# Kernel optimization log

Hardware: AMD Instinct MI355X
Metric: run time of the kernel (lower is better)

## Reference

```python
import jax, jax.numpy as jnp
import numpy as np

INV_SQRT2 = 0.7071067811865476
N, E, K, S = 10000, 120000, 8, 7
DE, DA, DT, DR, DC = 128, 128, 64, 16, 16
T = E * K

def act(x):
    return jax.nn.silu(x)

def residual_stack(x, Ws):
    # Ws: (n_layers, 2, D, D); GemNet ResidualLayer: two Dense+act, scaled skip
    for lw in Ws:
        y = act(act(x @ lw[0]) @ lw[1])
        x = (x + y) * INV_SQRT2
    return x

def bilinear(rbf_W1, sph, m, id_reduce, id_ragged, W):
    # EfficientInteractionBilinear (GemNet): ragged scatter into (E,Kmax,emb) then basis contractions
    m2 = jnp.zeros((rbf_W1.shape[0], sph.shape[1], m.shape[-1]), m.dtype)
    m2 = m2.at[id_reduce, id_ragged].set(m)          # (E, K, DT)
    sum_k = jnp.einsum('eks,ekc->esc', sph, m2)      # (E, S, DT)
    a = jnp.einsum('ejs,esc->ejc', rbf_W1, sum_k)    # (E, DC, DT)
    return jnp.einsum('ejc,cju->eu', a, W)           # (E, DT)

def _forward(h, m_st, rbf_h, rbf3, cbf_rbfW1, cbf_sph,
             W_mlp_st, W_m_kt, W_t_rbf, W_down, W_bil, W_st3, W_ts3,
             res_before, res_after, W_ae_rbf, W_ae_in, res_atom, W_asi, res_m,
             idx_s, idx_t, idx_swap, id3_kt, id3_st, id3_ragged_idx):
    x_skip = m_st @ W_mlp_st
    # --- TripletInteraction ---
    m_kt = act(m_st @ W_m_kt)
    m_kt = m_kt * (rbf3 @ W_t_rbf)        # scale_rbf == 1.0 (identity ScaleFactor)
    m_kt = act(m_kt @ W_down)             # (E, DT)
    xb = bilinear(cbf_rbfW1, cbf_sph, m_kt[id3_kt], id3_st, id3_ragged_idx, W_bil)
    x_st = act(xb @ W_st3)
    x_ts = act(xb @ W_ts3)[idx_swap]
    x3 = (x_st + x_ts) * INV_SQRT2
    # --- merge + residual stacks ---
    x = (x_skip + x3) * INV_SQRT2
    x = residual_stack(x, res_before)
    x = (x + m_st) * INV_SQRT2
    x = residual_stack(x, res_after)
    # --- AtomEmbedding: edge->atom scatter-add ---
    xa = x * (rbf_h @ W_ae_rbf)
    h2 = jax.ops.segment_sum(xa, idx_t, num_segments=h.shape[0])  # scale_sum == 1.0
    h_new = residual_stack(act(h2 @ W_ae_in), res_atom)
    # --- AtomSelfInteraction: gather-concat-Dense ---
    m = act(jnp.concatenate([h_new[idx_s], h_new[idx_t], x], axis=-1) @ W_asi)
    m = residual_stack(m, res_m)
    m = (m + x) * INV_SQRT2
    return h_new, m

def setup_inputs():
    key = jax.random.key(0)
    ks = jax.random.split(key, 24)
    def w(k, shape):
        return jax.random.normal(k, shape, jnp.float32) * (1.0 / np.sqrt(shape[-2]))
    return dict(
        h=jax.random.normal(ks[0], (N, DA), jnp.float32),
        m_st=jax.random.normal(ks[1], (E, DE), jnp.float32),
        rbf_h=jax.random.uniform(ks[2], (E, DR), jnp.float32),
        rbf3=jax.random.uniform(ks[3], (E, DR), jnp.float32),
        cbf_rbfW1=jax.random.normal(ks[4], (E, DC, S), jnp.float32) * 0.2,
        cbf_sph=jax.random.normal(ks[5], (E, K, S), jnp.float32) * 0.2,
        W_mlp_st=w(ks[6], (DE, DE)),
        W_m_kt=w(ks[7], (DE, DE)),
        W_t_rbf=w(ks[8], (DR, DE)),
        W_down=w(ks[9], (DE, DT)),
        W_bil=jax.random.normal(ks[10], (DT, DC, DT), jnp.float32) * (1.0 / np.sqrt(DT * DC)),
        W_st3=w(ks[11], (DT, DE)),
        W_ts3=w(ks[12], (DT, DE)),
        res_before=w(ks[13], (1, 2, DE, DE)),
        res_after=w(ks[14], (2, 2, DE, DE)),
        W_ae_rbf=w(ks[15], (DR, DE)),
        W_ae_in=w(ks[16], (DE, DA)),
        res_atom=w(ks[17], (2, 2, DA, DA)),
        W_asi=w(ks[18], (2 * DA + DE, DE)),
        res_m=w(ks[19], (2, 2, DE, DE)),
        idx_s=jax.random.randint(ks[20], (E,), 0, N, jnp.int32),
        idx_t=jax.random.randint(ks[21], (E,), 0, N, jnp.int32),
        idx_swap=jax.random.permutation(ks[22], E).astype(jnp.int32),
        id3_kt=jax.random.randint(ks[23], (T,), 0, E, jnp.int32),
        id3_st=jnp.repeat(jnp.arange(E, dtype=jnp.int32), K),
        id3_ragged_idx=jnp.tile(jnp.arange(K, dtype=jnp.int32), E),
    )

def reference(h, m_st, rbf_h, rbf3, cbf_rbfW1, cbf_sph,
              W_mlp_st, W_m_kt, W_t_rbf, W_down, W_bil, W_st3, W_ts3,
              res_before, res_after, W_ae_rbf, W_ae_in, res_atom, W_asi, res_m,
              idx_s, idx_t, idx_swap, id3_kt, id3_st, id3_ragged_idx):
    return _forward(h, m_st, rbf_h, rbf3, cbf_rbfW1, cbf_sph,
                    W_mlp_st, W_m_kt, W_t_rbf, W_down, W_bil, W_st3, W_ts3,
                    res_before, res_after, W_ae_rbf, W_ae_in, res_atom, W_asi, res_m,
                    idx_s, idx_t, idx_swap, id3_kt, id3_st, id3_ragged_idx)
```

## Files before the change

### kernel.cpp

```cpp
#include <hip/hip_runtime.h>


#define EE 120000
#define NA 10000

constexpr float C_INV = 0.70710678118654752440f;

using f32x4 = __attribute__((ext_vector_type(4))) float;
using f32x2 = __attribute__((ext_vector_type(2))) float;
using s16x8 = __attribute__((ext_vector_type(8))) short;
using s16x4 = __attribute__((ext_vector_type(4))) short;

__device__ __forceinline__ float act_silu(float x) { return x / (1.0f + __expf(-x)); }

__device__ __forceinline__ unsigned short f2bf(float f) {
    unsigned int u = __float_as_uint(f);
    u += 0x7fffu + ((u >> 16) & 1u);
    return (unsigned short)(u >> 16);
}
__device__ __forceinline__ float bf2f(unsigned short h) {
    return __uint_as_float(((unsigned int)h) << 16);
}
__device__ __forceinline__ unsigned int cvtpk(float a, float b) {
    unsigned int r;
    asm("v_cvt_pk_bf16_f32 %0, %1, %2" : "=v"(r) : "v"(a), "v"(b));
    return r;
}

template<int MT, int KQ>
__device__ __forceinline__ void load_w(const unsigned short* __restrict__ W, int KW,
                                       int l, s16x8 (&a)[MT][KQ])
{
    const int fr = l & 15;
    const int k8 = (l >> 4) << 3;
    #pragma unroll
    for (int mt = 0; mt < MT; ++mt)
        #pragma unroll
        for (int kq = 0; kq < KQ; ++kq)
            a[mt][kq] = *(const s16x8*)&W[(size_t)(mt * 16 + fr) * KW + kq * 32 + k8];
}

template<int MT, int NF, int KQ>
__device__ __forceinline__ void gemm_pre(
    const s16x8 (&a)[MT][KQ], const char* ldsB, int RS,
    int rowBase, int l, f32x4 (&acc)[MT][NF])
{
    const int fr = l & 15;
    const int k8 = (l >> 4) << 3;
    #pragma unroll
    for (int kq = 0; kq < KQ; ++kq) {
        s16x8 b[NF];
        #pragma unroll
        for (int nf = 0; nf < NF; ++nf) {
            const int row = rowBase + nf * 16 + fr;
            const int kb  = ((kq * 32 + k8) * 2) ^ ((row & 7) << 4);
            b[nf] = *(const s16x8*)(ldsB + row * RS + kb);
        }
        #pragma unroll
        for (int mt = 0; mt < MT; ++mt)
            #pragma unroll
            for (int nf = 0; nf < NF; ++nf)
                acc[mt][nf] = __builtin_amdgcn_mfma_f32_16x16x32_bf16(
                    a[mt][kq], b[nf], acc[mt][nf], 0, 0, 0);
    }
}

template<int MT, int NF>
__device__ __forceinline__ void zacc(f32x4 (&acc)[MT][NF])
{
    #pragma unroll
    for (int mt = 0; mt < MT; ++mt)
        #pragma unroll
        for (int nf = 0; nf < NF; ++nf)
            acc[mt][nf] = (f32x4){0.f, 0.f, 0.f, 0.f};
}

__device__ __forceinline__ void packA(char* lds, int RS, int row, int outF0, f32x4 v)
{
    uint2 p;
    p.x = cvtpk(v[0], v[1]);
    p.y = cvtpk(v[2], v[3]);
    *(uint2*)(lds + row * RS + ((outF0 * 2) ^ ((row & 7) << 4))) = p;
}

__device__ __forceinline__ void store_bf4(unsigned short* dst, f32x4 v)
{
    uint2 p;
    p.x = cvtpk(v[0], v[1]);
    p.y = cvtpk(v[2], v[3]);
    *(uint2*)dst = p;
}

template<int ROWS>
__device__ __forceinline__ void stage_f32(char* lds, const float* __restrict__ src,
                                          int row0, int M, int tid)
{
    #pragma unroll
    for (int u = 0; u < ROWS * 16 / 512; ++u) {
        const int flat = tid + u * 512;
        const int row  = flat >> 4;
        const int k8   = (flat & 15) << 3;
        const int grow = row0 + row;
        uint4 val = {0u, 0u, 0u, 0u};
        if (grow < M) {
            const float* p = src + (size_t)grow * 128 + k8;
            f32x4 lo = *(const f32x4*)p;
            f32x4 hi = *(const f32x4*)(p + 4);
            val.x = cvtpk(lo[0], lo[1]);
            val.y = cvtpk(lo[2], lo[3]);
            val.z = cvtpk(hi[0], hi[1]);
            val.w = cvtpk(hi[2], hi[3]);
        }
        *(uint4*)(lds + row * 256 + ((k8 * 2) ^ ((row & 7) << 4))) = val;
    }
}

template<bool MSTM, int NF>
__device__ __forceinline__ void res_layer(
    char* A, char* B,
    const unsigned short* W0, const unsigned short* W1,
    int wm, int wn, int l, f32x4 (&x)[2][NF],
    const s16x4 (*ms)[NF])
{
    const int fr = l & 15;
    const int fq = (l >> 4) << 2;

    s16x8 aw[2][4];
    load_w<2, 4>(W0 + (size_t)(wm * 32) * 128, 128, l, aw);
    f32x4 acc[2][NF];
    zacc(acc);
    gemm_pre<2, NF, 4>(aw, A, 256, wn * NF * 16, l, acc);

    s16x8 aw1[2][4];
    load_w<2, 4>(W1 + (size_t)(wm * 32) * 128, 128, l, aw1);

    #pragma unroll
    for (int mt = 0; mt < 2; ++mt)
        #pragma unroll
        for (int nf = 0; nf < NF; ++nf) {
            const int row = wn * NF * 16 + nf * 16 + fr;
            const int of0 = wm * 32 + mt * 16 + fq;
            f32x4 v;
            #pragma unroll
            for (int q = 0; q < 4; ++q) v[q] = act_silu(acc[mt][nf][q]);
            packA(B, 256, row, of0, v);
        }
    __syncthreads();

    zacc(acc);
    gemm_pre<2, NF, 4>(aw1, B, 256, wn * NF * 16, l, acc);
    #pragma unroll
    for (int mt = 0; mt < 2; ++mt)
        #pragma unroll
        for (int nf = 0; nf < NF; ++nf) {
            const int row = wn * NF * 16 + nf * 16 + fr;
            const int of0 = wm * 32 + mt * 16 + fq;
            #pragma unroll
            for (int q = 0; q < 4; ++q)
                x[mt][nf][q] = (x[mt][nf][q] + act_silu(acc[mt][nf][q])) * C_INV;
            if (MSTM) {
                #pragma unroll
                for (int q = 0; q < 4; ++q)
                    x[mt][nf][q] = (x[mt][nf][q] +
                                    bf2f((unsigned short)ms[mt][nf][q])) * C_INV;
            }
            packA(A, 256, row, of0, x[mt][nf]);
        }
    __syncthreads();
}

__device__ __forceinline__ s16x4 read_frag(const char* lds, int row, int of0)
{
    return *(const s16x4*)(lds + row * 256 + ((of0 * 2) ^ ((row & 7) << 4)));
}

__global__ __launch_bounds__(512, 4) void front_k(
    const float* __restrict__ m_st, const unsigned short* __restrict__ scale_b,
    const unsigned short* __restrict__ Wmkt, const unsigned short* __restrict__ Wdown,
    unsigned short* __restrict__ mkt_b)
{
    __shared__ char A[128 * 256];
    const int tid = threadIdx.x;
    const int l = tid & 63, w = tid >> 6, wm = w & 3, wn = w >> 2;
    const int fr = l & 15, fq = (l >> 4) << 2;
    const int row0 = blockIdx.x * 128;

    s16x8 aw[2][4];
    load_w<2, 4>(Wmkt + (size_t)(wm * 32) * 128, 128, l, aw);

    stage_f32<128>(A, m_st, row0, EE, tid);
    __syncthreads();

    f32x4 acc[2][4];
    zacc(acc);
    gemm_pre<2, 4, 4>(aw, A, 256, wn * 64, l, acc);

    s16x8 aw2[1][4];
    load_w<1, 4>(Wdown + (size_t)(wm * 16) * 128, 128, l, aw2);

    __syncthreads();
    #pragma unroll
    for (int mt = 0; mt < 2; ++mt)
        #pragma unroll
        for (int nf = 0; nf < 4; ++nf) {
            const int row = wn * 64 + nf * 16 + fr;
            const int grow = row0 + row;
            const int of0 = wm * 32 + mt * 16 + fq;
            f32x4 v = {0.f, 0.f, 0.f, 0.f};
            if (grow < EE) {
                s16x4 sc = *(const s16x4*)&scale_b[(size_t)grow * 128 + of0];
                #pragma unroll
                for (int q = 0; q < 4; ++q)
                    v[q] = act_silu(acc[mt][nf][q]) * bf2f((unsigned short)sc[q]);
            }
            packA(A, 256, row, of0, v);
        }
    __syncthreads();

    f32x4 acc2[1][4];
    zacc(acc2);
    gemm_pre<1, 4, 4>(aw2, A, 256, wn * 64, l, acc2);
    #pragma unroll
    for (int nf = 0; nf < 4; ++nf) {
        const int row = wn * 64 + nf * 16 + fr;
        const int grow = row0 + row;
        if (grow >= EE) continue;
        const int of0 = wm * 16 + fq;
        f32x4 v;
        #pragma unroll
        for (int q = 0; q < 4; ++q) v[q] = act_silu(acc2[0][nf][q]);
        store_bf4(&mkt_b[(size_t)grow * 64 + of0], v);
    }
}

__global__ __launch_bounds__(512, 4) void st3ts3_k(
    const unsigned short* __restrict__ xb_b,
    const unsigned short* __restrict__ Wst3, const unsigned short* __restrict__ Wts3,
    unsigned short* __restrict__ yst, unsigned short* __restrict__ yts)
{
    __shared__ char A[128 * 128];
    const int tid = threadIdx.x;
    const int l = tid & 63, w = tid >> 6, wm = w & 3, wn = w >> 2;
    const int fr = l & 15, fq = (l >> 4) << 2;
    const int row0 = blockIdx.x * 128;

    s16x8 awS[2][2], awT[2][2];
    load_w<2, 2>(Wst3 + (size_t)(wm * 32) * 64, 64, l, awS);
    load_w<2, 2>(Wts3 + (size_t)(wm * 32) * 64, 64, l, awT);

    #pragma unroll
    for (int u = 0; u < 2; ++u) {
        const int flat = tid + u * 512;
        const int row = flat >> 3;
        const int k8 = (flat & 7) << 3;
        const int grow = row0 + row;
        s16x8 v = {0, 0, 0, 0, 0, 0, 0, 0};
        if (grow < EE) v = *(const s16x8*)&xb_b[(size_t)grow * 64 + k8];
        *(s16x8*)(A + row * 128 + ((k8 * 2) ^ ((row & 7) << 4))) = v;
    }
    __syncthreads();

    f32x4 aS[2][4], aT[2][4];
    zacc(aS); zacc(aT);
    {
        const int k8 = (l >> 4) << 3;
        #pragma unroll
        for (int kq = 0; kq < 2; ++kq) {
            s16x8 b[4];
            #pragma unroll
            for (int nf = 0; nf < 4; ++nf) {
                const int row = wn * 64 + nf * 16 + fr;
                const int kb  = ((kq * 32 + k8) * 2) ^ ((row & 7) << 4);
                b[nf] = *(const s16x8*)(A + row * 128 + kb);
            }
            #pragma unroll
            for (int mt = 0; mt < 2; ++mt)
                #pragma unroll
                for (int nf = 0; nf < 4; ++nf) {
                    aS[mt][nf] = __builtin_amdgcn_mfma_f32_16x16x32_bf16(
                        awS[mt][kq], b[nf], aS[mt][nf], 0, 0, 0);
                    aT[mt][nf] = __builtin_amdgcn_mfma_f32_16x16x32_bf16(
                        awT[mt][kq], b[nf], aT[mt][nf], 0, 0, 0);
                }
        }
    }

    #pragma unroll
    for (int mt = 0; mt < 2; ++mt)
        #pragma unroll
        for (int nf = 0; nf < 4; ++nf) {
            const int row = wn * 64 + nf * 16 + fr;
            const int grow = row0 + row;
            if (grow >= EE) continue;
            const int of0 = wm * 32 + mt * 16 + fq;
            f32x4 vs, vt;
            #pragma unroll
            for (int q = 0; q < 4; ++q) {
                vs[q] = act_silu(aS[mt][nf][q]);
                vt[q] = act_silu(aT[mt][nf][q]);
            }
            store_bf4(&yst[(size_t)grow * 128 + of0], vs);
            store_bf4(&yts[(size_t)grow * 128 + of0], vt);
        }
}

__global__ __launch_bounds__(512, 4) void chain_k(
    const float* __restrict__ m_st,
    const unsigned short* __restrict__ yst, const unsigned short* __restrict__ yts,
    const int* __restrict__ idx_swap,
    const unsigned short* __restrict__ Wmlp,
    const unsigned short* __restrict__ Wrb0, const unsigned short* __restrict__ Wrb1,
    const unsigned short* __restrict__ Wra0, const unsigned short* __restrict__ Wra1,
    const unsigned short* __restrict__ Wra2, const unsigned short* __restrict__ Wra3,
    unsigned short* __restrict__ xb_out)
{
    __shared__ char A[128 * 256];
    __shared__ char B[128 * 256];
    const int tid = threadIdx.x;
    const int l = tid & 63, w = tid >> 6, wm = w & 3, wn = w >> 2;
    const int fr = l & 15, fq = (l >> 4) << 2;
    const int row0 = blockIdx.x * 128;

    s16x8 aw[2][4];
    load_w<2, 4>(Wmlp + (size_t)(wm * 32) * 128, 128, l, aw);

    stage_f32<128>(A, m_st, row0, EE, tid);
    __syncthreads();

    f32x4 acc[2][4];
    zacc(acc);
    gemm_pre<2, 4, 4>(aw, A, 256, wn * 64, l, acc);

    s16x4 ms[2][4];
    #pragma unroll
    for (int mt = 0; mt < 2; ++mt)
        #pragma unroll
        for (int nf = 0; nf < 4; ++nf)
            ms[mt][nf] = read_frag(A, wn * 64 + nf * 16 + fr, wm * 32 + mt * 16 + fq);

    f32x4 x[2][4];
    #pragma unroll
    for (int mt = 0; mt < 2; ++mt)
        #pragma unroll
        for (int nf = 0; nf < 4; ++nf) {
            const int row = wn * 64 + nf * 16 + fr;
            const int grow = row0 + row;
            const int of0 = wm * 32 + mt * 16 + fq;
            if (grow < EE) {
                s16x4 a = *(const s16x4*)&yst[(size_t)grow * 128 + of0];
                const int sw = idx_swap[grow];
                s16x4 b = *(const s16x4*)&yts[(size_t)sw * 128 + of0];
                #pragma unroll
                for (int q = 0; q < 4; ++q)
                    x[mt][nf][q] = (acc[mt][nf][q] +
                        (bf2f((unsigned short)a[q]) + bf2f((unsigned short)b[q])) * C_INV) * C_INV;
            } else {
                x[mt][nf] = (f32x4){0.f, 0.f, 0.f, 0.f};
            }
        }
    __syncthreads();
    #pragma unroll
    for (int mt = 0; mt < 2; ++mt)
        #pragma unroll
        for (int nf = 0; nf < 4; ++nf)
            packA(A, 256, wn * 64 + nf * 16 + fr, wm * 32 + mt * 16 + fq, x[mt][nf]);
    __syncthreads();

    res_layer<true , 4>(A, B, Wrb0, Wrb1, wm, wn, l, x, ms);
    res_layer<false, 4>(A, B, Wra0, Wra1, wm, wn, l, x, nullptr);
    res_layer<false, 4>(A, B, Wra2, Wra3, wm, wn, l, x, nullptr);

    #pragma unroll
    for (int mt = 0; mt < 2; ++mt)
        #pragma unroll
        for (int nf = 0; nf < 4; ++nf) {
            const int row = wn * 64 + nf * 16 + fr;
            const int grow = row0 + row;
            if (grow >= EE) continue;
            const int of0 = wm * 32 + mt * 16 + fq;
            store_bf4(&xb_out[(size_t)grow * 128 + of0], x[mt][nf]);
        }
}

__global__ __launch_bounds__(512, 4) void atom_k(
    const float* __restrict__ h2,
    const unsigned short* __restrict__ Wae,
    const unsigned short* __restrict__ Wr0, const unsigned short* __restrict__ Wr1,
    const unsigned short* __restrict__ Wr2, const unsigned short* __restrict__ Wr3,
    float* __restrict__ out_h, unsigned short* __restrict__ h_b)
{
    __shared__ char A[64 * 256];
    __shared__ char B[64 * 256];
    const int tid = threadIdx.x;
    const int l = tid & 63, w = tid >> 6, wm = w & 3, wn = w >> 2;
    const int fr = l & 15, fq = (l >> 4) << 2;
    const int row0 = blockIdx.x * 64;

    s16x8 aw[2][4];
    load_w<2, 4>(Wae + (size_t)(wm * 32) * 128, 128, l, aw);

    stage_f32<64>(A, h2, row0, NA, tid);
    __syncthreads();

    f32x4 acc[2][2];
    zacc(acc);
    gemm_pre<2, 2, 4>(aw, A, 256, wn * 32, l, acc);
    f32x4 x[2][2];
    #pragma unroll
    for (int mt = 0; mt < 2; ++mt)
        #pragma unroll
        for (int nf = 0; nf < 2; ++nf)
            #pragma unroll
            for (int q = 0; q < 4; ++q)
                x[mt][nf][q] = act_silu(acc[mt][nf][q]);
    __syncthreads();
    #pragma unroll
    for (int mt = 0; mt < 2; ++mt)
        #pragma unroll
        for (int nf = 0; nf < 2; ++nf)
            packA(A, 256, wn * 32 + nf * 16 + fr, wm * 32 + mt * 16 + fq, x[mt][nf]);
    __syncthreads();

    res_layer<false, 2>(A, B, Wr0, Wr1, wm, wn, l, x, nullptr);
    res_layer<false, 2>(A, B, Wr2, Wr3, wm, wn, l, x, nullptr);

    #pragma unroll
    for (int mt = 0; mt < 2; ++mt)
        #pragma unroll
        for (int nf = 0; nf < 2; ++nf) {
            const int row = wn * 32 + nf * 16 + fr;
            const int grow = row0 + row;
            if (grow >= NA) continue;
            const int of0 = wm * 32 + mt * 16 + fq;
            *(f32x4*)&out_h[(size_t)grow * 128 + of0] = x[mt][nf];
            store_bf4(&h_b[(size_t)grow * 128 + of0], x[mt][nf]);
        }
}

__global__ __launch_bounds__(512, 4) void asi_k(
    const unsigned short* __restrict__ h_b, const unsigned short* __restrict__ x_b,
    const int* __restrict__ idx_s, const int* __restrict__ idx_t,
    const unsigned short* __restrict__ Wasi,
    const unsigned short* __restrict__ Wm0, const unsigned short* __restrict__ Wm1,
    const unsigned short* __restrict__ Wm2, const unsigned short* __restrict__ Wm3,
    float* __restrict__ out_m)
{
    __shared__ char A[128 * 256];
    __shared__ char B[128 * 256];
    const int tid = threadIdx.x;
    const int l = tid & 63, w = tid >> 6, wm = w & 3, wn = w >> 2;
    const int fr = l & 15, fq = (l >> 4) << 2;
    const int row0 = blockIdx.x * 128;

    f32x4 acc[2][4];
    zacc(acc);

    for (int c = 0; c < 3; ++c) {
        s16x8 aw[2][4];
        load_w<2, 4>(Wasi + (size_t)(wm * 32) * 384 + c * 128, 384, l, aw);
        #pragma unroll
        for (int u = 0; u < 4; ++u) {
            const int flat = tid + u * 512;
            const int row = flat >> 4;
            const int k8 = (flat & 15) << 3;
            const int grow = row0 + row;
            s16x8 v = {0, 0, 0, 0, 0, 0, 0, 0};
            if (grow < EE) {
                const unsigned short* src =
                    (c == 0) ? h_b + (size_t)idx_s[grow] * 128
                  : (c == 1) ? h_b + (size_t)idx_t[grow] * 128
                             : x_b + (size_t)grow * 128;
                v = *(const s16x8*)&src[k8];
            }
            *(s16x8*)(A + row * 256 + ((k8 * 2) ^ ((row & 7) << 4))) = v;
        }
        __syncthreads();
        gemm_pre<2, 4, 4>(aw, A, 256, wn * 64, l, acc);
        __syncthreads();
    }

    f32x4 x[2][4];
    #pragma unroll
    for (int mt = 0; mt < 2; ++mt)
        #pragma unroll
        for (int nf = 0; nf < 4; ++nf)
            #pragma unroll
            for (int q = 0; q < 4; ++q)
                x[mt][nf][q] = act_silu(acc[mt][nf][q]);
    #pragma unroll
    for (int mt = 0; mt < 2; ++mt)
        #pragma unroll
        for (int nf = 0; nf < 4; ++nf)
            packA(A, 256, wn * 64 + nf * 16 + fr, wm * 32 + mt * 16 + fq, x[mt][nf]);
    __syncthreads();

    res_layer<false, 4>(A, B, Wm0, Wm1, wm, wn, l, x, nullptr);
    res_layer<false, 4>(A, B, Wm2, Wm3, wm, wn, l, x, nullptr);

    #pragma unroll
    for (int mt = 0; mt < 2; ++mt)
        #pragma unroll
        for (int nf = 0; nf < 4; ++nf) {
            const int row = wn * 64 + nf * 16 + fr;
            const int grow = row0 + row;
            if (grow >= EE) continue;
            const int of0 = wm * 32 + mt * 16 + fq;
            s16x4 xv = *(const s16x4*)&x_b[(size_t)grow * 128 + of0];
            f32x4 o;
            #pragma unroll
            for (int q = 0; q < 4; ++q)
                o[q] = (x[mt][nf][q] + bf2f((unsigned short)xv[q])) * C_INV;
            *(f32x4*)&out_m[(size_t)grow * 128 + of0] = o;
        }
}

__global__ __launch_bounds__(256) void rbf_scale_k(
    const float* __restrict__ A, const float* __restrict__ W,
    unsigned short* __restrict__ out, int M)
{
    __shared__ float Ws[16][128];
    const int tid = threadIdx.x;
    #pragma unroll
    for (int t = tid; t < 512; t += 256) {
        int kk = t >> 5, c4 = (t & 31) << 2;
        *(float4*)&Ws[kk][c4] = *(const float4*)(W + kk * 128 + c4);
    }
    __syncthreads();
    const int tx = tid & 31, ty = tid >> 5;
    const int row0 = blockIdx.x * 128;
    #pragma unroll
    for (int i = 0; i < 16; ++i) {
        const int row = row0 + ty + i * 8;
        if (row >= M) continue;
        float av[16];
        #pragma unroll
        for (int j = 0; j < 4; ++j) {
            float4 a = *(const float4*)(A + (size_t)row * 16 + j * 4);
            av[j * 4] = a.x; av[j * 4 + 1] = a.y; av[j * 4 + 2] = a.z; av[j * 4 + 3] = a.w;
        }
        f32x4 s = {0.f, 0.f, 0.f, 0.f};
        #pragma unroll
        for (int k = 0; k < 16; ++k) {
            float4 wv = *(const float4*)&Ws[k][tx * 4];
            s[0] += av[k] * wv.x; s[1] += av[k] * wv.y;
            s[2] += av[k] * wv.z; s[3] += av[k] * wv.w;
        }
        store_bf4(&out[(size_t)row * 128 + tx * 4], s);
    }
}

__global__ void hist_k(const int* __restrict__ idxt, int* __restrict__ cnt)
{
    int i = blockIdx.x * 256 + threadIdx.x;
    if (i < EE) atomicAdd(&cnt[idxt[i]], 1);
}

__global__ __launch_bounds__(256) void scan_k(const int* __restrict__ cnt,
                                              int* __restrict__ start, int* __restrict__ wrk)
{
    __shared__ int ps[256];
    const int t = threadIdx.x;
    int s = 0;
    for (int j = 0; j < 40; ++j) {
        int idx = t * 40 + j;
        if (idx < NA) s += cnt[idx];
    }
    ps[t] = s;
    __syncthreads();
    for (int off = 1; off < 256; off <<= 1) {
        int v = (t >= off) ? ps[t - off] : 0;
        __syncthreads();
        ps[t] += v;
        __syncthreads();
    }
    int run = ps[t] - s;
    for (int j = 0; j < 40; ++j) {
        int idx = t * 40 + j;
        if (idx < NA) {
            start[idx] = run;
            wrk[idx] = run;
            run += cnt[idx];
        }
    }
    if (t == 255) start[NA] = ps[255];
}

__global__ void place_k(const int* __restrict__ idxt, int* __restrict__ wrk,
                        int* __restrict__ order)
{
    int i = blockIdx.x * 256 + threadIdx.x;
    if (i < EE) {
        int pos = atomicAdd(&wrk[idxt[i]], 1);
        order[pos] = i;
    }
}

__global__ __launch_bounds__(256) void segsum_k(
    const unsigned short* __restrict__ x_b, const float* __restrict__ rbf_h,
    const float* __restrict__ Wae, const int* __restrict__ start,
    const int* __restrict__ order, float* __restrict__ h2)
{
    const int tid = threadIdx.x;
    const int l = tid & 63, w = tid >> 6;
    const int a = blockIdx.x * 4 + w;
    if (a >= NA) return;

    float wc[32];
    #pragma unroll
    for (int j = 0; j < 16; ++j) {
        f32x2 v = *(const f32x2*)(Wae + j * 128 + 2 * l);
        wc[2 * j] = v[0]; wc[2 * j + 1] = v[1];
    }

    const int s = start[a], e_end = start[a + 1];
    float acc0 = 0.f, acc1 = 0.f;
    for (int i = s; i < e_end; ++i) {
        const int e = __builtin_amdgcn_readfirstlane(order[i]);
        const unsigned int xv = *(const unsigned int*)(x_b + (size_t)e * 128 + 2 * l);
        const float* rp = rbf_h + (size_t)e * 16;
        float c0 = 0.f, c1 = 0.f;
        #pragma unroll
        for (int j = 0; j < 16; ++j) {
            float r = rp[j];
            c0 += r * wc[2 * j];
            c1 += r * wc[2 * j + 1];
        }
        acc0 += bf2f((unsigned short)(xv & 0xffff)) * c0;
        acc1 += bf2f((unsigned short)(xv >> 16)) * c1;
    }
    f32x2 o; o[0] = acc0; o[1] = acc1;
    *(f32x2*)&h2[(size_t)a * 128 + 2 * l] = o;
}

__global__ void wconv_k(const float* __restrict__ Wbil, unsigned short* __restrict__ WT)
{
    int t = blockIdx.x * 256 + threadIdx.x;
    int u = t >> 10, k = t & 1023, j = k >> 6, c = k & 63;
    WT[t] = f2bf(Wbil[(size_t)(c * 16 + j) * 64 + u]);
}

struct WDesc { const float* src; int K; int N; int off; };
struct WTab  { WDesc d[21]; };

__global__ void wconvall_k(WTab tab, unsigned short* __restrict__ dst)
{
    WDesc d = tab.d[blockIdx.x];
    const int tot = d.K * d.N;
    for (int i = threadIdx.x; i < tot; i += 256) {
        int n = i / d.K, k = i - n * d.K;
        dst[d.off + i] = f2bf(d.src[(size_t)k * d.N + n]);
    }
}

__device__ __forceinline__ float rlc(const f32x4& cv, int idx, int lbase)
{
    const int c = idx & 3;
    float comp = (c == 0) ? cv[0] : (c == 1) ? cv[1] : (c == 2) ? cv[2] : cv[3];
    return __uint_as_float(__builtin_amdgcn_readlane(__float_as_uint(comp),
                                                     lbase + (idx >> 2)));
}

__global__ __launch_bounds__(512) void bilinear3_k(
    const unsigned short* __restrict__ mkt,
    const float* __restrict__ rbfW1,
    const float* __restrict__ sph,
    const int*   __restrict__ id3kt,
    const unsigned short* __restrict__ WT,
    unsigned short* __restrict__ xb)
{
    __shared__ unsigned short aS[32 * 1024];
    float* pS = (float*)aS;

    const int tid = threadIdx.x;
    const int l   = tid & 63;
    const int w   = tid >> 6;
    const int e0  = blockIdx.x * 32;

    s16x8 bfrag[4][4];
    {
        const int u  = l & 15;
        const int kh = w * 128 + ((l >> 4) << 3);
        #pragma unroll
        for (int nt = 0; nt < 4; ++nt)
            #pragma unroll
            for (int kq = 0; kq < 4; ++kq)
                bfrag[nt][kq] = *(const s16x8*)&WT[(size_t)(nt * 16 + u) * 1024 + kh + kq * 32];
    }

    #pragma unroll
    for (int r = 0; r < 4; ++r) {
        const int eL = r * 8 + w;
        const int eG = e0 + eL;

        f32x4 cv = {0.f, 0.f, 0.f, 0.f};
        if (l < 14)       cv = *(const f32x4*)(sph   + (size_t)eG * 56  + l * 4);
        else if (l < 42)  cv = *(const f32x4*)(rbfW1 + (size_t)eG * 112 + (l - 14) * 4);

        float m2r[8];
        #pragma unroll
        for (int k = 0; k < 8; ++k)
            m2r[k] = bf2f(mkt[(size_t)id3kt[eG * 8 + k] * 64 + l]);

        float sk[7] = {0.f, 0.f, 0.f, 0.f, 0.f, 0.f, 0.f};
        #pragma unroll
        for (int k = 0; k < 8; ++k)
            #pragma unroll
            for (int s = 0; s < 7; ++s)
                sk[s] += rlc(cv, k * 7 + s, 0) * m2r[k];

        unsigned short* arow = aS + eL * 1024;
        const int lsw = l ^ ((eL & 7) << 3);
        #pragma unroll
        for (int j = 0; j < 16; ++j) {
            float av = 0.f;
            #pragma unroll
            for (int s = 0; s < 7; ++s)
                av += rlc(cv, j * 7 + s, 14) * sk[s];
            arow[j * 64 + lsw] = f2bf(av);
        }
    }
    __syncthreads();

    f32x4 acc[2][4];
    #pragma unroll
    for (int mt = 0; mt < 2; ++mt)
        #pragma unroll
        for (int nt = 0; nt < 4; ++nt)
            acc[mt][nt] = (f32x4){0.f, 0.f, 0.f, 0.f};

    const int kbase = w * 128 + ((l >> 4) << 3);
    #pragma unroll
    for (int kq = 0; kq < 4; ++kq) {
        s16x8 afr[2];
        #pragma unroll
        for (int mt = 0; mt < 2; ++mt) {
            const int row = mt * 16 + (l & 15);
            const int kk  = (kbase + kq * 32) ^ ((row & 7) << 3);
            afr[mt] = *(const s16x8*)&aS[row * 1024 + kk];
        }
        #pragma unroll
        for (int mt = 0; mt < 2; ++mt)
            #pragma unroll
            for (int nt = 0; nt < 4; ++nt)
                acc[mt][nt] = __builtin_amdgcn_mfma_f32_16x16x32_bf16(
                    afr[mt], bfrag[nt][kq], acc[mt][nt], 0, 0, 0);
    }
    __syncthreads();

    #pragma unroll
    for (int mt = 0; mt < 2; ++mt)
        #pragma unroll
        for (int nt = 0; nt < 4; ++nt)
            #pragma unroll
            for (int q = 0; q < 4; ++q) {
                const int e = mt * 16 + ((l >> 4) << 2) + q;
                const int u = nt * 16 + (l & 15);
                pS[(w * 32 + e) * 64 + u] = acc[mt][nt][q];
            }
    __syncthreads();

    {
        const int e  = tid >> 4;
        const int u0 = (tid & 15) << 2;
        f32x4 s = (f32x4){0.f, 0.f, 0.f, 0.f};
        #pragma unroll
        for (int ww = 0; ww < 8; ++ww)
            s += *(const f32x4*)&pS[(ww * 32 + e) * 64 + u0];
        store_bf4(&xb[(size_t)(e0 + e) * 64 + u0], s);
    }
}

extern "C" void kernel_launch(void* const* d_in, const int* in_sizes, int n_in,
                              void* d_out, int out_size, void* d_ws, size_t ws_size,
                              hipStream_t stream)
{
    const float* m_st      = (const float*)d_in[1];
    const float* rbf_h     = (const float*)d_in[2];
    const float* rbf3      = (const float*)d_in[3];
    const float* cbf_rbfW1 = (const float*)d_in[4];
    const float* cbf_sph   = (const float*)d_in[5];
    const float* W_mlp_st  = (const float*)d_in[6];
    const float* W_m_kt    = (const float*)d_in[7];
    const float* W_t_rbf   = (const float*)d_in[8];
    const float* W_down    = (const float*)d_in[9];
    const float* W_bil     = (const float*)d_in[10];
    const float* W_st3     = (const float*)d_in[11];
    const float* W_ts3     = (const float*)d_in[12];
    const float* resb      = (const float*)d_in[13];
    const float* resa      = (const float*)d_in[14];
    const float* W_ae_rbf  = (const float*)d_in[15];
    const float* W_ae_in   = (const float*)d_in[16];
    const float* resat     = (const float*)d_in[17];
    const float* W_asi     = (const float*)d_in[18];
    const float* resm      = (const float*)d_in[19];
    const int*   idx_s     = (const int*)d_in[20];
    const int*   idx_t     = (const int*)d_in[21];
    const int*   idx_swap  = (const int*)d_in[22];
    const int*   id3_kt    = (const int*)d_in[23];

    float* h2 = (float*)d_ws;
    unsigned short* scale_b = (unsigned short*)(h2 + (size_t)NA * 128);
    unsigned short* yst_b   = scale_b;
    unsigned short* yts_b   = scale_b + (size_t)EE * 128;
    unsigned short* x_b     = yts_b + (size_t)EE * 128;
    unsigned short* mkt_b   = x_b + (size_t)EE * 128;
    unsigned short* xb_b    = mkt_b + (size_t)EE * 64;
    unsigned short* h_b     = xb_b + (size_t)EE * 64;
    unsigned short* WTbil   = h_b + (size_t)NA * 128;
    unsigned short* WTall   = WTbil + 65536;
    int* cnt   = (int*)(WTall + 352256);
    int* start = cnt + NA;
    int* wrk   = start + NA + 1;
    int* order = wrk + NA;

    float* out_h = (float*)d_out;
    float* out_m = out_h + (size_t)NA * 128;

    const dim3 blk(256);
    const dim3 blk5(512);
    const int gE  = (EE + 127) / 128;
    const int gN64 = (NA + 63) / 64;
    constexpr size_t SQ = 128 * 128;

    WTab tab; int off = 0; int oi = 0;
    auto put = [&](const float* s, int K, int N) {
        int o = off; tab.d[oi].src = s; tab.d[oi].K = K; tab.d[oi].N = N;
        tab.d[oi].off = o; ++oi; off += K * N; return o;
    };
    const int o_mlp  = put(W_mlp_st, 128, 128);
    const int o_mktw = put(W_m_kt, 128, 128);
    const int o_down = put(W_down, 128, 64);
    const int o_st3  = put(W_st3, 64, 128);
    const int o_ts3  = put(W_ts3, 64, 128);
    const int o_rb0  = put(resb, 128, 128);
    const int o_rb1  = put(resb + SQ, 128, 128);
    const int o_ra0  = put(resa, 128, 128);
    const int o_ra1  = put(resa + SQ, 128, 128);
    const int o_ra2  = put(resa + 2 * SQ, 128, 128);
    const int o_ra3  = put(resa + 3 * SQ, 128, 128);
    const int o_aein = put(W_ae_in, 128, 128);
    const int o_rat0 = put(resat, 128, 128);
    const int o_rat1 = put(resat + SQ, 128, 128);
    const int o_rat2 = put(resat + 2 * SQ, 128, 128);
    const int o_rat3 = put(resat + 3 * SQ, 128, 128);
    const int o_asi  = put(W_asi, 384, 128);
    const int o_rm0  = put(resm, 128, 128);
    const int o_rm1  = put(resm + SQ, 128, 128);
    const int o_rm2  = put(resm + 2 * SQ, 128, 128);
    const int o_rm3  = put(resm + 3 * SQ, 128, 128);

    hipMemsetAsync(cnt, 0, NA * sizeof(int), stream);
    wconv_k<<<65536 / 256, blk, 0, stream>>>(W_bil, WTbil);
    wconvall_k<<<21, blk, 0, stream>>>(tab, WTall);
    hist_k<<<(EE + 255) / 256, blk, 0, stream>>>(idx_t, cnt);
    scan_k<<<1, blk, 0, stream>>>(cnt, start, wrk);
    place_k<<<(EE + 255) / 256, blk, 0, stream>>>(idx_t, wrk, order);

    rbf_scale_k<<<gE, blk, 0, stream>>>(rbf3, W_t_rbf, scale_b, EE);
    front_k<<<gE, blk5, 0, stream>>>(m_st, scale_b, WTall + o_mktw, WTall + o_down, mkt_b);
    bilinear3_k<<<EE / 32, blk5, 0, stream>>>(
        mkt_b, cbf_rbfW1, cbf_sph, id3_kt, WTbil, xb_b);
    st3ts3_k<<<gE, blk5, 0, stream>>>(xb_b, WTall + o_st3, WTall + o_ts3, yst_b, yts_b);
    chain_k<<<gE, blk5, 0, stream>>>(
        m_st, yst_b, yts_b, idx_swap,
        WTall + o_mlp, WTall + o_rb0, WTall + o_rb1,
        WTall + o_ra0, WTall + o_ra1, WTall + o_ra2, WTall + o_ra3,
        x_b);
    segsum_k<<<(NA + 3) / 4, blk, 0, stream>>>(x_b, rbf_h, W_ae_rbf, start, order, h2);
    atom_k<<<gN64, blk5, 0, stream>>>(
        h2, WTall + o_aein,
        WTall + o_rat0, WTall + o_rat1, WTall + o_rat2, WTall + o_rat3,
        out_h, h_b);
    asi_k<<<gE, blk5, 0, stream>>>(
        h_b, x_b, idx_s, idx_t,
        WTall + o_asi,
        WTall + o_rm0, WTall + o_rm1, WTall + o_rm2, WTall + o_rm3,
        out_m);
}
```

Baseline: 701.7 us.

## Halve row tiles, raise occupancy, and restructure bilinear kernel with scalar coefficient loads

Most edge kernels (front, st3ts3, chain, asi) now process 64 rows per block instead of 128, with half the LDS and accumulators, and request 8 blocks per CU in their launch bounds. This should raise occupancy and latency hiding. The bilinear kernel now handles 16 edges per block. It reads the sph and rbf coefficients through wave-uniform scalar addresses instead of readlane, and loads W_bil fragments from global memory inside the MFMA loop instead of holding them in registers. In exchange there are twice as many blocks and weight-fragment loads per row, and the tighter register budget risks spills.

```diff
diff --git a/kernel.cpp b/kernel.cpp
--- a/kernel.cpp
+++ b/kernel.cpp
@@ -174,26 +174,26 @@
     return *(const s16x4*)(lds + row * 256 + ((of0 * 2) ^ ((row & 7) << 4)));
 }
 
-__global__ __launch_bounds__(512, 4) void front_k(
+__global__ __launch_bounds__(512, 8) void front_k(
     const float* __restrict__ m_st, const unsigned short* __restrict__ scale_b,
     const unsigned short* __restrict__ Wmkt, const unsigned short* __restrict__ Wdown,
     unsigned short* __restrict__ mkt_b)
 {
-    __shared__ char A[128 * 256];
+    __shared__ char A[64 * 256];
     const int tid = threadIdx.x;
     const int l = tid & 63, w = tid >> 6, wm = w & 3, wn = w >> 2;
     const int fr = l & 15, fq = (l >> 4) << 2;
-    const int row0 = blockIdx.x * 128;
+    const int row0 = blockIdx.x * 64;
 
     s16x8 aw[2][4];
     load_w<2, 4>(Wmkt + (size_t)(wm * 32) * 128, 128, l, aw);
 
-    stage_f32<128>(A, m_st, row0, EE, tid);
-    __syncthreads();
-
-    f32x4 acc[2][4];
+    stage_f32<64>(A, m_st, row0, EE, tid);
+    __syncthreads();
+
+    f32x4 acc[2][2];
     zacc(acc);
-    gemm_pre<2, 4, 4>(aw, A, 256, wn * 64, l, acc);
+    gemm_pre<2, 2, 4>(aw, A, 256, wn * 32, l, acc);
 
     s16x8 aw2[1][4];
     load_w<1, 4>(Wdown + (size_t)(wm * 16) * 128, 128, l, aw2);
@@ -202,8 +202,8 @@
     #pragma unroll
     for (int mt = 0; mt < 2; ++mt)
         #pragma unroll
-        for (int nf = 0; nf < 4; ++nf) {
-            const int row = wn * 64 + nf * 16 + fr;
+        for (int nf = 0; nf < 2; ++nf) {
+            const int row = wn * 32 + nf * 16 + fr;
             const int grow = row0 + row;
             const int of0 = wm * 32 + mt * 16 + fq;
             f32x4 v = {0.f, 0.f, 0.f, 0.f};
@@ -217,12 +217,12 @@
         }
     __syncthreads();
 
-    f32x4 acc2[1][4];
+    f32x4 acc2[1][2];
     zacc(acc2);
-    gemm_pre<1, 4, 4>(aw2, A, 256, wn * 64, l, acc2);
-    #pragma unroll
-    for (int nf = 0; nf < 4; ++nf) {
-        const int row = wn * 64 + nf * 16 + fr;
+    gemm_pre<1, 2, 4>(aw2, A, 256, wn * 32, l, acc2);
+    #pragma unroll
+    for (int nf = 0; nf < 2; ++nf) {
+        const int row = wn * 32 + nf * 16 + fr;
         const int grow = row0 + row;
         if (grow >= EE) continue;
         const int of0 = wm * 16 + fq;
@@ -233,26 +233,24 @@
     }
 }
 
-__global__ __launch_bounds__(512, 4) void st3ts3_k(
+__global__ __launch_bounds__(512, 8) void st3ts3_k(
     const unsigned short* __restrict__ xb_b,
     const unsigned short* __restrict__ Wst3, const unsigned short* __restrict__ Wts3,
     unsigned short* __restrict__ yst, unsigned short* __restrict__ yts)
 {
-    __shared__ char A[128 * 128];
+    __shared__ char A[64 * 128];
     const int tid = threadIdx.x;
     const int l = tid & 63, w = tid >> 6, wm = w & 3, wn = w >> 2;
     const int fr = l & 15, fq = (l >> 4) << 2;
-    const int row0 = blockIdx.x * 128;
+    const int row0 = blockIdx.x * 64;
 
     s16x8 awS[2][2], awT[2][2];
     load_w<2, 2>(Wst3 + (size_t)(wm * 32) * 64, 64, l, awS);
     load_w<2, 2>(Wts3 + (size_t)(wm * 32) * 64, 64, l, awT);
 
-    #pragma unroll
-    for (int u = 0; u < 2; ++u) {
-        const int flat = tid + u * 512;
-        const int row = flat >> 3;
-        const int k8 = (flat & 7) << 3;
+    {
+        const int row = tid >> 3;
+        const int k8 = (tid & 7) << 3;
         const int grow = row0 + row;
         s16x8 v = {0, 0, 0, 0, 0, 0, 0, 0};
         if (grow < EE) v = *(const s16x8*)&xb_b[(size_t)grow * 64 + k8];
@@ -260,23 +258,23 @@
     }
     __syncthreads();
 
-    f32x4 aS[2][4], aT[2][4];
+    f32x4 aS[2][2], aT[2][2];
     zacc(aS); zacc(aT);
     {
         const int k8 = (l >> 4) << 3;
         #pragma unroll
         for (int kq = 0; kq < 2; ++kq) {
-            s16x8 b[4];
-            #pragma unroll
-            for (int nf = 0; nf < 4; ++nf) {
-                const int row = wn * 64 + nf * 16 + fr;
+            s16x8 b[2];
+            #pragma unroll
+            for (int nf = 0; nf < 2; ++nf) {
+                const int row = wn * 32 + nf * 16 + fr;
                 const int kb  = ((kq * 32 + k8) * 2) ^ ((row & 7) << 4);
                 b[nf] = *(const s16x8*)(A + row * 128 + kb);
             }
             #pragma unroll
             for (int mt = 0; mt < 2; ++mt)
                 #pragma unroll
-                for (int nf = 0; nf < 4; ++nf) {
+                for (int nf = 0; nf < 2; ++nf) {
                     aS[mt][nf] = __builtin_amdgcn_mfma_f32_16x16x32_bf16(
                         awS[mt][kq], b[nf], aS[mt][nf], 0, 0, 0);
                     aT[mt][nf] = __builtin_amdgcn_mfma_f32_16x16x32_bf16(
@@ -288,8 +286,8 @@
     #pragma unroll
     for (int mt = 0; mt < 2; ++mt)
         #pragma unroll
-        for (int nf = 0; nf < 4; ++nf) {
-            const int row = wn * 64 + nf * 16 + fr;
+        for (int nf = 0; nf < 2; ++nf) {
+            const int row = wn * 32 + nf * 16 + fr;
             const int grow = row0 + row;
             if (grow >= EE) continue;
             const int of0 = wm * 32 + mt * 16 + fq;
@@ -304,7 +302,7 @@
         }
 }
 
-__global__ __launch_bounds__(512, 4) void chain_k(
+__global__ __launch_bounds__(512, 8) void chain_k(
     const float* __restrict__ m_st,
     const unsigned short* __restrict__ yst, const unsigned short* __restrict__ yts,
     const int* __restrict__ idx_swap,
@@ -314,36 +312,36 @@
     const unsigned short* __restrict__ Wra2, const unsigned short* __restrict__ Wra3,
     unsigned short* __restrict__ xb_out)
 {
-    __shared__ char A[128 * 256];
-    __shared__ char B[128 * 256];
+    __shared__ char A[64 * 256];
+    __shared__ char B[64 * 256];
     const int tid = threadIdx.x;
     const int l = tid & 63, w = tid >> 6, wm = w & 3, wn = w >> 2;
     const int fr = l & 15, fq = (l >> 4) << 2;
-    const int row0 = blockIdx.x * 128;
+    const int row0 = blockIdx.x * 64;
 
     s16x8 aw[2][4];
     load_w<2, 4>(Wmlp + (size_t)(wm * 32) * 128, 128, l, aw);
 
-    stage_f32<128>(A, m_st, row0, EE, tid);
-    __syncthreads();
-
-    f32x4 acc[2][4];
+    stage_f32<64>(A, m_st, row0, EE, tid);
+    __syncthreads();
+
+    f32x4 acc[2][2];
     zacc(acc);
-    gemm_pre<2, 4, 4>(aw, A, 256, wn * 64, l, acc);
-
-    s16x4 ms[2][4];
-    #pragma unroll
-    for (int mt = 0; mt < 2; ++mt)
-        #pragma unroll
-        for (int nf = 0; nf < 4; ++nf)
-            ms[mt][nf] = read_frag(A, wn * 64 + nf * 16 + fr, wm * 32 + mt * 16 + fq);
-
-    f32x4 x[2][4];
-    #pragma unroll
-    for (int mt = 0; mt < 2; ++mt)
-        #pragma unroll
-        for (int nf = 0; nf < 4; ++nf) {
-            const int row = wn * 64 + nf * 16 + fr;
+    gemm_pre<2, 2, 4>(aw, A, 256, wn * 32, l, acc);
+
+    s16x4 ms[2][2];
+    #pragma unroll
+    for (int mt = 0; mt < 2; ++mt)
+        #pragma unroll
+        for (int nf = 0; nf < 2; ++nf)
+            ms[mt][nf] = read_frag(A, wn * 32 + nf * 16 + fr, wm * 32 + mt * 16 + fq);
+
+    f32x4 x[2][2];
+    #pragma unroll
+    for (int mt = 0; mt < 2; ++mt)
+        #pragma unroll
+        for (int nf = 0; nf < 2; ++nf) {
+            const int row = wn * 32 + nf * 16 + fr;
             const int grow = row0 + row;
             const int of0 = wm * 32 + mt * 16 + fq;
             if (grow < EE) {
@@ -362,19 +360,19 @@
     #pragma unroll
     for (int mt = 0; mt < 2; ++mt)
         #pragma unroll
-        for (int nf = 0; nf < 4; ++nf)
-            packA(A, 256, wn * 64 + nf * 16 + fr, wm * 32 + mt * 16 + fq, x[mt][nf]);
-    __syncthreads();
-
-    res_layer<true , 4>(A, B, Wrb0, Wrb1, wm, wn, l, x, ms);
-    res_layer<false, 4>(A, B, Wra0, Wra1, wm, wn, l, x, nullptr);
-    res_layer<false, 4>(A, B, Wra2, Wra3, wm, wn, l, x, nullptr);
-
-    #pragma unroll
-    for (int mt = 0; mt < 2; ++mt)
-        #pragma unroll
-        for (int nf = 0; nf < 4; ++nf) {
-            const int row = wn * 64 + nf * 16 + fr;
+        for (int nf = 0; nf < 2; ++nf)
+            packA(A, 256, wn * 32 + nf * 16 + fr, wm * 32 + mt * 16 + fq, x[mt][nf]);
+    __syncthreads();
+
+    res_layer<true , 2>(A, B, Wrb0, Wrb1, wm, wn, l, x, ms);
+    res_layer<false, 2>(A, B, Wra0, Wra1, wm, wn, l, x, nullptr);
+    res_layer<false, 2>(A, B, Wra2, Wra3, wm, wn, l, x, nullptr);
+
+    #pragma unroll
+    for (int mt = 0; mt < 2; ++mt)
+        #pragma unroll
+        for (int nf = 0; nf < 2; ++nf) {
+            const int row = wn * 32 + nf * 16 + fr;
             const int grow = row0 + row;
             if (grow >= EE) continue;
             const int of0 = wm * 32 + mt * 16 + fq;
@@ -382,7 +380,7 @@
         }
 }
 
-__global__ __launch_bounds__(512, 4) void atom_k(
+__global__ __launch_bounds__(512, 8) void atom_k(
     const float* __restrict__ h2,
     const unsigned short* __restrict__ Wae,
     const unsigned short* __restrict__ Wr0, const unsigned short* __restrict__ Wr1,
@@ -437,7 +435,7 @@
         }
 }
 
-__global__ __launch_bounds__(512, 4) void asi_k(
+__global__ __launch_bounds__(512, 8) void asi_k(
     const unsigned short* __restrict__ h_b, const unsigned short* __restrict__ x_b,
     const int* __restrict__ idx_s, const int* __restrict__ idx_t,
     const unsigned short* __restrict__ Wasi,
@@ -445,21 +443,21 @@
     const unsigned short* __restrict__ Wm2, const unsigned short* __restrict__ Wm3,
     float* __restrict__ out_m)
 {
-    __shared__ char A[128 * 256];
-    __shared__ char B[128 * 256];
+    __shared__ char A[64 * 256];
+    __shared__ char B[64 * 256];
     const int tid = threadIdx.x;
     const int l = tid & 63, w = tid >> 6, wm = w & 3, wn = w >> 2;
     const int fr = l & 15, fq = (l >> 4) << 2;
-    const int row0 = blockIdx.x * 128;
-
-    f32x4 acc[2][4];
+    const int row0 = blockIdx.x * 64;
+
+    f32x4 acc[2][2];
     zacc(acc);
 
     for (int c = 0; c < 3; ++c) {
         s16x8 aw[2][4];
         load_w<2, 4>(Wasi + (size_t)(wm * 32) * 384 + c * 128, 384, l, aw);
         #pragma unroll
-        for (int u = 0; u < 4; ++u) {
+        for (int u = 0; u < 2; ++u) {
             const int flat = tid + u * 512;
             const int row = flat >> 4;
             const int k8 = (flat & 15) << 3;
@@ -475,33 +473,33 @@
             *(s16x8*)(A + row * 256 + ((k8 * 2) ^ ((row & 7) << 4))) = v;
         }
         __syncthreads();
-        gemm_pre<2, 4, 4>(aw, A, 256, wn * 64, l, acc);
+        gemm_pre<2, 2, 4>(aw, A, 256, wn * 32, l, acc);
         __syncthreads();
     }
 
-    f32x4 x[2][4];
-    #pragma unroll
-    for (int mt = 0; mt < 2; ++mt)
-        #pragma unroll
-        for (int nf = 0; nf < 4; ++nf)
+    f32x4 x[2][2];
+    #pragma unroll
+    for (int mt = 0; mt < 2; ++mt)
+        #pragma unroll
+        for (int nf = 0; nf < 2; ++nf)
             #pragma unroll
             for (int q = 0; q < 4; ++q)
                 x[mt][nf][q] = act_silu(acc[mt][nf][q]);
     #pragma unroll
     for (int mt = 0; mt < 2; ++mt)
         #pragma unroll
-        for (int nf = 0; nf < 4; ++nf)
-            packA(A, 256, wn * 64 + nf * 16 + fr, wm * 32 + mt * 16 + fq, x[mt][nf]);
-    __syncthreads();
-
-    res_layer<false, 4>(A, B, Wm0, Wm1, wm, wn, l, x, nullptr);
-    res_layer<false, 4>(A, B, Wm2, Wm3, wm, wn, l, x, nullptr);
-
-    #pragma unroll
-    for (int mt = 0; mt < 2; ++mt)
-        #pragma unroll
-        for (int nf = 0; nf < 4; ++nf) {
-            const int row = wn * 64 + nf * 16 + fr;
+        for (int nf = 0; nf < 2; ++nf)
+            packA(A, 256, wn * 32 + nf * 16 + fr, wm * 32 + mt * 16 + fq, x[mt][nf]);
+    __syncthreads();
+
+    res_layer<false, 2>(A, B, Wm0, Wm1, wm, wn, l, x, nullptr);
+    res_layer<false, 2>(A, B, Wm2, Wm3, wm, wn, l, x, nullptr);
+
+    #pragma unroll
+    for (int mt = 0; mt < 2; ++mt)
+        #pragma unroll
+        for (int nf = 0; nf < 2; ++nf) {
+            const int row = wn * 32 + nf * 16 + fr;
             const int grow = row0 + row;
             if (grow >= EE) continue;
             const int of0 = wm * 32 + mt * 16 + fq;
@@ -652,15 +650,7 @@
     }
 }
 
-__device__ __forceinline__ float rlc(const f32x4& cv, int idx, int lbase)
-{
-    const int c = idx & 3;
-    float comp = (c == 0) ? cv[0] : (c == 1) ? cv[1] : (c == 2) ? cv[2] : cv[3];
-    return __uint_as_float(__builtin_amdgcn_readlane(__float_as_uint(comp),
-                                                     lbase + (idx >> 2)));
-}
-
-__global__ __launch_bounds__(512) void bilinear3_k(
+__global__ __launch_bounds__(512, 8) void bilinear4_k(
     const unsigned short* __restrict__ mkt,
     const float* __restrict__ rbfW1,
     const float* __restrict__ sph,
@@ -668,45 +658,34 @@
     const unsigned short* __restrict__ WT,
     unsigned short* __restrict__ xb)
 {
-    __shared__ unsigned short aS[32 * 1024];
+    __shared__ unsigned short aS[16 * 1024];
     float* pS = (float*)aS;
 
     const int tid = threadIdx.x;
     const int l   = tid & 63;
     const int w   = tid >> 6;
-    const int e0  = blockIdx.x * 32;
-
-    s16x8 bfrag[4][4];
-    {
-        const int u  = l & 15;
-        const int kh = w * 128 + ((l >> 4) << 3);
-        #pragma unroll
-        for (int nt = 0; nt < 4; ++nt)
-            #pragma unroll
-            for (int kq = 0; kq < 4; ++kq)
-                bfrag[nt][kq] = *(const s16x8*)&WT[(size_t)(nt * 16 + u) * 1024 + kh + kq * 32];
-    }
-
-    #pragma unroll
-    for (int r = 0; r < 4; ++r) {
+    const int e0  = blockIdx.x * 16;
+
+    #pragma unroll
+    for (int r = 0; r < 2; ++r) {
         const int eL = r * 8 + w;
-        const int eG = e0 + eL;
-
-        f32x4 cv = {0.f, 0.f, 0.f, 0.f};
-        if (l < 14)       cv = *(const f32x4*)(sph   + (size_t)eG * 56  + l * 4);
-        else if (l < 42)  cv = *(const f32x4*)(rbfW1 + (size_t)eG * 112 + (l - 14) * 4);
+        const int eU = __builtin_amdgcn_readfirstlane(e0 + eL);
+
+        const int*   idU = id3kt + (size_t)eU * 8;
+        const float* spU = sph   + (size_t)eU * 56;
+        const float* rbU = rbfW1 + (size_t)eU * 112;
 
         float m2r[8];
         #pragma unroll
         for (int k = 0; k < 8; ++k)
-            m2r[k] = bf2f(mkt[(size_t)id3kt[eG * 8 + k] * 64 + l]);
+            m2r[k] = bf2f(mkt[(size_t)idU[k] * 64 + l]);
 
         float sk[7] = {0.f, 0.f, 0.f, 0.f, 0.f, 0.f, 0.f};
         #pragma unroll
         for (int k = 0; k < 8; ++k)
             #pragma unroll
             for (int s = 0; s < 7; ++s)
-                sk[s] += rlc(cv, k * 7 + s, 0) * m2r[k];
+                sk[s] += spU[k * 7 + s] * m2r[k];
 
         unsigned short* arow = aS + eL * 1024;
         const int lsw = l ^ ((eL & 7) << 3);
@@ -715,58 +694,50 @@
             float av = 0.f;
             #pragma unroll
             for (int s = 0; s < 7; ++s)
-                av += rlc(cv, j * 7 + s, 14) * sk[s];
+                av += rbU[j * 7 + s] * sk[s];
             arow[j * 64 + lsw] = f2bf(av);
         }
     }
     __syncthreads();
 
-    f32x4 acc[2][4];
-    #pragma unroll
-    for (int mt = 0; mt < 2; ++mt)
-        #pragma unroll
-        for (int nt = 0; nt < 4; ++nt)
-            acc[mt][nt] = (f32x4){0.f, 0.f, 0.f, 0.f};
-
+    f32x4 acc[4];
+    #pragma unroll
+    for (int nt = 0; nt < 4; ++nt) acc[nt] = (f32x4){0.f, 0.f, 0.f, 0.f};
+
+    const int u16   = l & 15;
     const int kbase = w * 128 + ((l >> 4) << 3);
     #pragma unroll
     for (int kq = 0; kq < 4; ++kq) {
-        s16x8 afr[2];
-        #pragma unroll
-        for (int mt = 0; mt < 2; ++mt) {
-            const int row = mt * 16 + (l & 15);
-            const int kk  = (kbase + kq * 32) ^ ((row & 7) << 3);
-            afr[mt] = *(const s16x8*)&aS[row * 1024 + kk];
-        }
-        #pragma unroll
-        for (int mt = 0; mt < 2; ++mt)
-            #pragma unroll
-            for (int nt = 0; nt < 4; ++nt)
-                acc[mt][nt] = __builtin_amdgcn_mfma_f32_16x16x32_bf16(
-                    afr[mt], bfrag[nt][kq], acc[mt][nt], 0, 0, 0);
-    }
-    __syncthreads();
-
-    #pragma unroll
-    for (int mt = 0; mt < 2; ++mt)
-        #pragma unroll
-        for (int nt = 0; nt < 4; ++nt)
-            #pragma unroll
-            for (int q = 0; q < 4; ++q) {
-                const int e = mt * 16 + ((l >> 4) << 2) + q;
-                const int u = nt * 16 + (l & 15);
-                pS[(w * 32 + e) * 64 + u] = acc[mt][nt][q];
-            }
+        const int row = l & 15;
+        const int kk  = (kbase + kq * 32) ^ ((row & 7) << 3);
+        s16x8 afr = *(const s16x8*)&aS[row * 1024 + kk];
+        #pragma unroll
+        for (int nt = 0; nt < 4; ++nt) {
+            s16x8 bfr = *(const s16x8*)&WT[(size_t)(nt * 16 + u16) * 1024 + kbase + kq * 32];
+            acc[nt] = __builtin_amdgcn_mfma_f32_16x16x32_bf16(afr, bfr, acc[nt], 0, 0, 0);
+        }
+    }
+    __syncthreads();
+
+    #pragma unroll
+    for (int nt = 0; nt < 4; ++nt)
+        #pragma unroll
+        for (int q = 0; q < 4; ++q) {
+            const int e = ((l >> 4) << 2) + q;
+            const int u = nt * 16 + (l & 15);
+            pS[(w * 16 + e) * 64 + u] = acc[nt][q];
+        }
     __syncthreads();
 
     {
-        const int e  = tid >> 4;
-        const int u0 = (tid & 15) << 2;
-        f32x4 s = (f32x4){0.f, 0.f, 0.f, 0.f};
+        const int e  = tid >> 5;
+        const int u0 = (tid & 31) << 1;
+        f32x2 s = (f32x2){0.f, 0.f};
         #pragma unroll
         for (int ww = 0; ww < 8; ++ww)
-            s += *(const f32x4*)&pS[(ww * 32 + e) * 64 + u0];
-        store_bf4(&xb[(size_t)(e0 + e) * 64 + u0], s);
+            s += *(const f32x2*)&pS[(ww * 16 + e) * 64 + u0];
+        unsigned int pk = cvtpk(s[0], s[1]);
+        *(unsigned int*)&xb[(size_t)(e0 + e) * 64 + u0] = pk;
     }
 }
 
@@ -818,8 +789,9 @@
 
     const dim3 blk(256);
     const dim3 blk5(512);
-    const int gE  = (EE + 127) / 128;
-    const int gN64 = (NA + 63) / 64;
+    const int gE128 = (EE + 127) / 128;
+    const int gE64  = (EE + 63) / 64;
+    const int gN64  = (NA + 63) / 64;
     constexpr size_t SQ = 128 * 128;
 
     WTab tab; int off = 0; int oi = 0;
@@ -856,12 +828,12 @@
     scan_k<<<1, blk, 0, stream>>>(cnt, start, wrk);
     place_k<<<(EE + 255) / 256, blk, 0, stream>>>(idx_t, wrk, order);
 
-    rbf_scale_k<<<gE, blk, 0, stream>>>(rbf3, W_t_rbf, scale_b, EE);
-    front_k<<<gE, blk5, 0, stream>>>(m_st, scale_b, WTall + o_mktw, WTall + o_down, mkt_b);
-    bilinear3_k<<<EE / 32, blk5, 0, stream>>>(
+    rbf_scale_k<<<gE128, blk, 0, stream>>>(rbf3, W_t_rbf, scale_b, EE);
+    front_k<<<gE64, blk5, 0, stream>>>(m_st, scale_b, WTall + o_mktw, WTall + o_down, mkt_b);
+    bilinear4_k<<<EE / 16, blk5, 0, stream>>>(
         mkt_b, cbf_rbfW1, cbf_sph, id3_kt, WTbil, xb_b);
-    st3ts3_k<<<gE, blk5, 0, stream>>>(xb_b, WTall + o_st3, WTall + o_ts3, yst_b, yts_b);
-    chain_k<<<gE, blk5, 0, stream>>>(
+    st3ts3_k<<<gE64, blk5, 0, stream>>>(xb_b, WTall + o_st3, WTall + o_ts3, yst_b, yts_b);
+    chain_k<<<gE64, blk5, 0, stream>>>(
         m_st, yst_b, yts_b, idx_swap,
         WTall + o_mlp, WTall + o_rb0, WTall + o_rb1,
         WTall + o_ra0, WTall + o_ra1, WTall + o_ra2, WTall + o_ra3,
@@ -871,7 +843,7 @@
         h2, WTall + o_aein,
         WTall + o_rat0, WTall + o_rat1, WTall + o_rat2, WTall + o_rat3,
         out_h, h_b);
-    asi_k<<<gE, blk5, 0, stream>>>(
+    asi_k<<<gE64, blk5, 0, stream>>>(
         h_b, x_b, idx_s, idx_t,
         WTall + o_asi,
         WTall + o_rm0, WTall + o_rm1, WTall + o_rm2, WTall + o_rm3,
```

Result: slower. 790.0 us (+12.6%).
